# Kernel optimization log

Hardware: AMD Instinct MI355X
Metric: run time of the kernel (lower is better)

## Reference

```python
import jax, jax.numpy as jnp
import numpy as np

N_HEADS = 16
D_MODEL = 1024
D_HEAD = D_MODEL // N_HEADS


def setup_inputs() -> dict:
    key = jax.random.key(0)
    ks = jax.random.split(key, 5)
    scale = 0.02
    x = jax.random.normal(ks[0], (2, 2048, D_MODEL), dtype=jnp.float32)
    # torch.nn.Linear weights: (out_features, in_features)
    w_in = jax.random.normal(ks[1], (3 * D_MODEL, D_MODEL), dtype=jnp.float32) * scale
    b_in = jax.random.normal(ks[2], (3 * D_MODEL,), dtype=jnp.float32) * scale
    w_out = jax.random.normal(ks[3], (D_MODEL, D_MODEL), dtype=jnp.float32) * scale
    b_out = jax.random.normal(ks[4], (D_MODEL,), dtype=jnp.float32) * scale
    return {"x": x, "w_in": w_in, "b_in": b_in, "w_out": w_out, "b_out": b_out}


def reference(x, w_in, b_in, w_out, b_out):
    B, S, D = x.shape
    H, Dh = N_HEADS, D_HEAD
    qkv = x @ w_in.T + b_in                      # [B,S,3D]
    q, k, v = jnp.split(qkv, 3, axis=-1)
    q = q.reshape(B, S, H, Dh).transpose(0, 2, 1, 3)  # [B,H,S,Dh]
    k = k.reshape(B, S, H, Dh).transpose(0, 2, 1, 3)
    v = v.reshape(B, S, H, Dh).transpose(0, 2, 1, 3)
    scores = jnp.einsum('bhqd,bhkd->bhqk', q, k) / jnp.sqrt(jnp.float32(Dh))
    weights = jax.nn.softmax(scores, axis=-1)
    out = jnp.einsum('bhqk,bhkd->bhqd', weights, v)   # [B,H,S,Dh]
    # Faithful to original: reshape WITHOUT transposing heads back
    out = out.reshape(B, S, D)
    return out @ w_out.T + b_out
```

## Files before the change

kernel.cpp:

```cpp
#include <hip/hip_runtime.h>
#include <math.h>

constexpr int D_MODEL = 1024;
constexpr int N_HEADS = 16;
constexpr int D_HEAD  = 64;
constexpr int SEQ     = 2048;
constexpr int BATCH   = 2;
constexpr int M_ROWS  = BATCH * SEQ;
constexpr int QKV_N   = 3 * D_MODEL;
constexpr int KDIM    = 1024;
constexpr int NROWS   = BATCH * N_HEADS * SEQ;

typedef __bf16 bf16x8 __attribute__((ext_vector_type(8)));
typedef float  f32x4  __attribute__((ext_vector_type(4)));
typedef float  f32x16 __attribute__((ext_vector_type(16)));
typedef unsigned uint2v __attribute__((ext_vector_type(2)));

union U4 { uint4 u; bf16x8 b; ushort s[8]; };
union U2 { uint2 u; ushort s[4]; };

__device__ __forceinline__ unsigned pk2bf(float lo, float hi) {
    union { unsigned u; __bf16 b[2]; } cv;
    cv.b[0] = (__bf16)lo; cv.b[1] = (__bf16)hi;
    return cv.u;
}
__device__ __forceinline__ ushort f2bf(float f) {
    union { ushort s[2]; __bf16 b[2]; } cv;
    cv.b[0] = (__bf16)f;
    return cv.s[0];
}

__device__ __forceinline__ int swz(int row, int bytecol) {
    return row * 128 + (bytecol ^ ((row & 7) << 4));
}

__device__ __forceinline__ void gload16(const void* g, void* l) {
    __builtin_amdgcn_global_load_lds(
        (const __attribute__((address_space(1))) unsigned int*)g,
        (__attribute__((address_space(3))) unsigned int*)l, 16, 0, 0);
}

#define QSCALE 0.18033688011112042f

__global__ __launch_bounds__(256)
void convert3_kernel(const float* __restrict__ x,  ushort* __restrict__ xo,
                     const float* __restrict__ wi, ushort* __restrict__ wio,
                     const float* __restrict__ wo, ushort* __restrict__ woo) {
    const int na = M_ROWS * D_MODEL;
    const int nb = QKV_N * D_MODEL;
    const int nc = D_MODEL * D_MODEL;
    const int total = (na + nb + nc) / 8;
    for (int g = blockIdx.x * blockDim.x + threadIdx.x; g < total;
         g += gridDim.x * blockDim.x) {
        const int i = g * 8;
        const float* src; ushort* dst; int off;
        if (i < na)           { src = x;  dst = xo;  off = i; }
        else if (i < na + nb) { src = wi; dst = wio; off = i - na; }
        else                  { src = wo; dst = woo; off = i - na - nb; }
        const float4 a = *reinterpret_cast<const float4*>(src + off);
        const float4 b = *reinterpret_cast<const float4*>(src + off + 4);
        uint4 o;
        o.x = pk2bf(a.x, a.y); o.y = pk2bf(a.z, a.w);
        o.z = pk2bf(b.x, b.y); o.w = pk2bf(b.z, b.w);
        *reinterpret_cast<uint4*>(dst + off) = o;
    }
}

__device__ __forceinline__ void mfma_gemm_bt_128(
    const ushort* __restrict__ Ag, const ushort* __restrict__ Bg,
    int m0, int n0, ushort* As, ushort* Bs, f32x4 (&acc)[4][4])
{
    const int tid = threadIdx.x;
    const int l   = tid & 63;
    const int rl  = l & 15, hh = l >> 4;
    const int w   = tid >> 6;
    const int wm  = (w >> 1) * 64, wn = (w & 1) * 64;

    const int r0 = tid >> 2;
    const int ce = (tid & 3) * 8;
    const ushort* gA0 = Ag + (size_t)(m0 + r0) * KDIM + ce;
    const ushort* gA1 = gA0 + (size_t)64 * KDIM;
    const ushort* gB0 = Bg + (size_t)(n0 + r0) * KDIM + ce;
    const ushort* gB1 = gB0 + (size_t)64 * KDIM;
    char* lA = (char*)As + tid * 16;
    char* lB = (char*)Bs + tid * 16;

    for (int k0 = 0; k0 < KDIM; k0 += 32) {
        __syncthreads();
        gload16(gA0 + k0, lA);
        gload16(gA1 + k0, lA + 4096);
        gload16(gB0 + k0, lB);
        gload16(gB1 + k0, lB + 4096);
        __syncthreads();

        bf16x8 af[4], bf_[4];
        #pragma unroll
        for (int f = 0; f < 4; ++f)
            af[f]  = *(const bf16x8*)((const char*)As + (wm + f * 16 + rl) * 64 + hh * 16);
        #pragma unroll
        for (int f = 0; f < 4; ++f)
            bf_[f] = *(const bf16x8*)((const char*)Bs + (wn + f * 16 + rl) * 64 + hh * 16);
        #pragma unroll
        for (int i = 0; i < 4; ++i)
            #pragma unroll
            for (int j = 0; j < 4; ++j)
                acc[i][j] = __builtin_amdgcn_mfma_f32_16x16x32_bf16(af[i], bf_[j], acc[i][j], 0, 0, 0);
    }
}

__global__ __launch_bounds__(256)
void qkv_mfma_kernel(const ushort* __restrict__ xb, const ushort* __restrict__ wb,
                     const float* __restrict__ b_in,
                     ushort* __restrict__ Q, ushort* __restrict__ K, ushort* __restrict__ V) {
    __shared__ __align__(16) ushort As[128 * 32];
    __shared__ __align__(16) ushort Bs[128 * 32];

    f32x4 acc[4][4];
    #pragma unroll
    for (int i = 0; i < 4; ++i)
        #pragma unroll
        for (int j = 0; j < 4; ++j) acc[i][j] = (f32x4){0.f, 0.f, 0.f, 0.f};

    const int m0 = blockIdx.y * 128, n0 = blockIdx.x * 128;
    mfma_gemm_bt_128(xb, wb, m0, n0, As, Bs, acc);

    const int l  = threadIdx.x & 63, w = threadIdx.x >> 6;
    const int rl = l & 15, hh = l >> 4;
    const int mb = m0 + (w >> 1) * 64, nb = n0 + (w & 1) * 64;

    #pragma unroll
    for (int j = 0; j < 4; ++j) {
        const int n  = nb + j * 16 + rl;
        const float bias = b_in[n];
        const int t  = n >> 10;
        const int jj = n & 1023;
        const int h  = jj >> 6;
        const int d  = jj & 63;
        ushort* dst = (t == 0) ? Q : (t == 1) ? K : V;
        const float sc = (t == 0) ? QSCALE : 1.0f;
        #pragma unroll
        for (int i = 0; i < 4; ++i)
            #pragma unroll
            for (int r = 0; r < 4; ++r) {
                const int m = mb + i * 16 + hh * 4 + r;
                const int b = m >> 11;
                const int s = m & (SEQ - 1);
                dst[((size_t)(b * N_HEADS + h) * SEQ + s) * D_HEAD + d] =
                    f2bf((acc[i][j][r] + bias) * sc);
            }
    }
}

__global__ __launch_bounds__(512)
void attn_mfma_split_kernel(const ushort* __restrict__ Q, const ushort* __restrict__ K,
                            const ushort* __restrict__ V, ushort* __restrict__ Op,
                            float* __restrict__ lbuf) {
    __shared__ __align__(16) char Ks[2][64 * 128];
    __shared__ __align__(16) char Vs[2][64 * 128];

    const int tid = threadIdx.x;
    const int w   = tid >> 6;
    const int l   = tid & 63;
    const int l31 = l & 31;
    const int lh  = l >> 5;

    const int bid  = blockIdx.x;
    const int nid  = (bid & 7) * 64 + (bid >> 3);
    const int bh   = nid >> 4;
    const int rem  = nid & 15;
    const int half = rem >> 3;
    const int qt   = rem & 7;

    const size_t base  = (size_t)bh * SEQ * D_HEAD;
    const size_t kbase = base + (size_t)half * 1024 * D_HEAD;
    const int qbase = qt * 256 + w * 32;

    bf16x8 qf[4];
    {
        const ushort* qp = Q + base + (size_t)(qbase + l31) * D_HEAD + lh * 8;
        #pragma unroll
        for (int c = 0; c < 4; ++c) {
            U4 t; t.u = *(const uint4*)(qp + c * 16);
            qf[c] = t.b;
        }
    }

    f32x16 ot0, ot1;
    #pragma unroll
    for (int r = 0; r < 16; ++r) { ot0[r] = 0.f; ot1[r] = 0.f; }
    float l_run = 0.0f;

    const int sr  = tid >> 3, seg = tid & 7;
    const int kp  = (tid & 31) * 2, dc = (tid >> 5) * 4;
    const ushort* gK  = K + kbase + (size_t)sr * D_HEAD + seg * 8;
    const ushort* gV0 = V + kbase + (size_t)kp * D_HEAD + dc;
    const ushort* gV1 = gV0 + D_HEAD;

    uint4 ka; U2 va, vb;
    ka   = *(const uint4*)(gK);
    va.u = *(const uint2*)(gV0);
    vb.u = *(const uint2*)(gV1);
    {
        char* kd = Ks[0]; char* vd = Vs[0];
        *(uint4*)(kd + swz(sr, seg * 16)) = ka;
        #pragma unroll
        for (int i = 0; i < 4; ++i) {
            const int d = dc + i;
            *(unsigned*)(vd + d * 128 + ((kp * 2) ^ ((d & 7) << 4))) =
                (unsigned)va.s[i] | ((unsigned)vb.s[i] << 16);
        }
    }

    constexpr int NT = 1024 / 64;
    for (int t = 0; t < NT; ++t) {
        const int cur = t & 1;
        __syncthreads();

        if (t + 1 < NT) {
            const size_t off = (size_t)(t + 1) * 64 * D_HEAD;
            ka   = *(const uint4*)(gK + off);
            va.u = *(const uint2*)(gV0 + off);
            vb.u = *(const uint2*)(gV1 + off);
        }
        const char* kbuf = Ks[cur];
        const char* vbuf = Vs[cur];

        f32x16 st0, st1;
        #pragma unroll
        for (int r = 0; r < 16; ++r) { st0[r] = 0.f; st1[r] = 0.f; }
        #pragma unroll
        for (int c = 0; c < 4; ++c) {
            const bf16x8 kf0 = *(const bf16x8*)(kbuf + swz(l31,      c * 32 + lh * 16));
            st0 = __builtin_amdgcn_mfma_f32_32x32x16_bf16(kf0, qf[c], st0, 0, 0, 0);
            const bf16x8 kf1 = *(const bf16x8*)(kbuf + swz(32 + l31, c * 32 + lh * 16));
            st1 = __builtin_amdgcn_mfma_f32_32x32x16_bf16(kf1, qf[c], st1, 0, 0, 0);
        }

        float ps = 0.f;
        #pragma unroll
        for (int r = 0; r < 16; ++r) {
            st0[r] = __builtin_amdgcn_exp2f(st0[r]); ps += st0[r];
            st1[r] = __builtin_amdgcn_exp2f(st1[r]); ps += st1[r];
        }
        l_run += ps;

        bf16x8 paf[4];
        #pragma unroll
        for (int t32 = 0; t32 < 2; ++t32) {
            const f32x16& s = t32 ? st1 : st0;
            const unsigned q0 = pk2bf(s[0],  s[1]);
            const unsigned q1 = pk2bf(s[2],  s[3]);
            const unsigned q2 = pk2bf(s[4],  s[5]);
            const unsigned q3 = pk2bf(s[6],  s[7]);
            const unsigned q4 = pk2bf(s[8],  s[9]);
            const unsigned q5 = pk2bf(s[10], s[11]);
            const unsigned q6 = pk2bf(s[12], s[13]);
            const unsigned q7 = pk2bf(s[14], s[15]);
            const uint2v x = __builtin_amdgcn_permlane32_swap(q0, q2, false, false);
            const uint2v y = __builtin_amdgcn_permlane32_swap(q1, q3, false, false);
            const uint2v z = __builtin_amdgcn_permlane32_swap(q4, q6, false, false);
            const uint2v u = __builtin_amdgcn_permlane32_swap(q5, q7, false, false);
            U4 f0; f0.u.x = x[0]; f0.u.y = y[0]; f0.u.z = x[1]; f0.u.w = y[1];
            U4 f1; f1.u.x = z[0]; f1.u.y = u[0]; f1.u.z = z[1]; f1.u.w = u[1];
            paf[t32 * 2]     = f0.b;
            paf[t32 * 2 + 1] = f1.b;
        }

        #pragma unroll
        for (int kc = 0; kc < 4; ++kc) {
            const bf16x8 vf0 = *(const bf16x8*)(vbuf + swz(l31,      kc * 32 + lh * 16));
            ot0 = __builtin_amdgcn_mfma_f32_32x32x16_bf16(vf0, paf[kc], ot0, 0, 0, 0);
            const bf16x8 vf1 = *(const bf16x8*)(vbuf + swz(32 + l31, kc * 32 + lh * 16));
            ot1 = __builtin_amdgcn_mfma_f32_32x32x16_bf16(vf1, paf[kc], ot1, 0, 0, 0);
        }

        if (t + 1 < NT) {
            char* kd = Ks[cur ^ 1]; char* vd = Vs[cur ^ 1];
            *(uint4*)(kd + swz(sr, seg * 16)) = ka;
            #pragma unroll
            for (int i = 0; i < 4; ++i) {
                const int d = dc + i;
                *(unsigned*)(vd + d * 128 + ((kp * 2) ^ ((d & 7) << 4))) =
                    (unsigned)va.s[i] | ((unsigned)vb.s[i] << 16);
            }
        }
    }

    l_run += __shfl_xor(l_run, 32, 64);
    const size_t grow = (size_t)bh * SEQ + qbase + l31;
    ushort* op = Op + ((size_t)half * NROWS + grow) * D_HEAD;
    #pragma unroll
    for (int dt = 0; dt < 2; ++dt) {
        const f32x16& o = dt ? ot1 : ot0;
        #pragma unroll
        for (int g = 0; g < 4; ++g) {
            const int d0 = dt * 32 + g * 8 + lh * 4;
            uint2 s2;
            s2.x = pk2bf(o[g * 4 + 0], o[g * 4 + 1]);
            s2.y = pk2bf(o[g * 4 + 2], o[g * 4 + 3]);
            *(uint2*)(op + d0) = s2;
        }
    }
    if (lh == 0) lbuf[(size_t)half * NROWS + grow] = l_run;
}

__global__ __launch_bounds__(256)
void combine_kernel(const ushort* __restrict__ Op, const float* __restrict__ lbuf,
                    ushort* __restrict__ A) {
    const int idx = blockIdx.x * 256 + threadIdx.x;
    const int row = idx >> 3;
    const int dc  = (idx & 7) * 8;
    const float inv = 1.0f / (lbuf[row] + lbuf[NROWS + row]);
    U4 o1, o2;
    o1.u = *(const uint4*)(Op + (size_t)row * D_HEAD + dc);
    o2.u = *(const uint4*)(Op + ((size_t)NROWS + row) * D_HEAD + dc);
    uint4 r;
    float v[8];
    #pragma unroll
    for (int i = 0; i < 8; ++i)
        v[i] = ((float)o1.b[i] + (float)o2.b[i]) * inv;
    r.x = pk2bf(v[0], v[1]); r.y = pk2bf(v[2], v[3]);
    r.z = pk2bf(v[4], v[5]); r.w = pk2bf(v[6], v[7]);
    *(uint4*)(A + (size_t)row * D_HEAD + dc) = r;
}

__global__ __launch_bounds__(256)
void out_mfma_kernel(const ushort* __restrict__ Ab, const ushort* __restrict__ wb,
                     const float* __restrict__ b_out, float* __restrict__ out) {
    __shared__ __align__(16) ushort As[128 * 32];
    __shared__ __align__(16) ushort Bs[128 * 32];

    f32x4 acc[4][4];
    #pragma unroll
    for (int i = 0; i < 4; ++i)
        #pragma unroll
        for (int j = 0; j < 4; ++j) acc[i][j] = (f32x4){0.f, 0.f, 0.f, 0.f};

    const int m0 = blockIdx.y * 128, n0 = blockIdx.x * 128;
    mfma_gemm_bt_128(Ab, wb, m0, n0, As, Bs, acc);

    const int l  = threadIdx.x & 63, w = threadIdx.x >> 6;
    const int rl = l & 15, hh = l >> 4;
    const int mb = m0 + (w >> 1) * 64, nb = n0 + (w & 1) * 64;

    #pragma unroll
    for (int j = 0; j < 4; ++j) {
        const int n = nb + j * 16 + rl;
        const float bias = b_out[n];
        #pragma unroll
        for (int i = 0; i < 4; ++i)
            #pragma unroll
            for (int r = 0; r < 4; ++r) {
                const int m = mb + i * 16 + hh * 4 + r;
                out[(size_t)m * D_MODEL + n] = acc[i][j][r] + bias;
            }
    }
}

extern "C" void kernel_launch(void* const* d_in, const int* in_sizes, int n_in,
                              void* d_out, int out_size, void* d_ws, size_t ws_size,
                              hipStream_t stream) {
    const float* x     = (const float*)d_in[0];
    const float* w_in  = (const float*)d_in[1];
    const float* b_in  = (const float*)d_in[2];
    const float* w_out = (const float*)d_in[3];
    const float* b_out = (const float*)d_in[4];
    float* out = (float*)d_out;

    const size_t T = (size_t)BATCH * N_HEADS * SEQ * D_HEAD;
    ushort* Qw  = (ushort*)d_ws;
    ushort* Kw  = Qw + T;
    ushort* Vw  = Kw + T;
    ushort* Opw = Vw + T;
    ushort* xb  = Opw + T;
    ushort* wib = xb + T;
    ushort* wob = wib + (size_t)QKV_N * D_MODEL;
    float*  lw  = (float*)(wob + (size_t)D_MODEL * D_MODEL);
    ushort* Aw  = Qw;

    convert3_kernel<<<2048, 256, 0, stream>>>(x, xb, w_in, wib, w_out, wob);

    qkv_mfma_kernel<<<dim3(QKV_N / 128, M_ROWS / 128), 256, 0, stream>>>(
        xb, wib, b_in, Qw, Kw, Vw);
    attn_mfma_split_kernel<<<512, 512, 0, stream>>>(Qw, Kw, Vw, Opw, lw);
    combine_kernel<<<NROWS * 8 / 256, 256, 0, stream>>>(Opw, lw, Aw);
    out_mfma_kernel<<<dim3(D_MODEL / 128, M_ROWS / 128), 256, 0, stream>>>(
        Aw, wob, b_out, out);
}
```

Before: 125.3 us.

## Fuse split-attention combine into output GEMM and interleave softmax with PV MFMAs

Removes the separate combine kernel. The output projection GEMM now loads both partial attention outputs, normalizes them by the summed row denominators, and writes the result straight into its shared-memory A tile, with the next tile prefetched into registers. This drops one launch and one round trip of the attention output through global memory, but each GEMM block repeats the combine work for its tile and issues extra loads. Inside the attention loop, the exp and PV MFMAs for the two 32-key halves are interleaved with s_setprio hints so that VALU work on one half can overlap the matrix ops on the other.

```diff
diff --git a/kernel.cpp b/kernel.cpp
--- a/kernel.cpp
+++ b/kernel.cpp
@@ -228,51 +228,103 @@
         f32x16 st0, st1;
         #pragma unroll
         for (int r = 0; r < 16; ++r) { st0[r] = 0.f; st1[r] = 0.f; }
+        __builtin_amdgcn_s_setprio(1);
         #pragma unroll
         for (int c = 0; c < 4; ++c) {
-            const bf16x8 kf0 = *(const bf16x8*)(kbuf + swz(l31,      c * 32 + lh * 16));
+            const bf16x8 kf0 = *(const bf16x8*)(kbuf + swz(l31, c * 32 + lh * 16));
             st0 = __builtin_amdgcn_mfma_f32_32x32x16_bf16(kf0, qf[c], st0, 0, 0, 0);
+        }
+        #pragma unroll
+        for (int c = 0; c < 4; ++c) {
             const bf16x8 kf1 = *(const bf16x8*)(kbuf + swz(32 + l31, c * 32 + lh * 16));
             st1 = __builtin_amdgcn_mfma_f32_32x32x16_bf16(kf1, qf[c], st1, 0, 0, 0);
         }
-
-        float ps = 0.f;
-        #pragma unroll
-        for (int r = 0; r < 16; ++r) {
-            st0[r] = __builtin_amdgcn_exp2f(st0[r]); ps += st0[r];
-            st1[r] = __builtin_amdgcn_exp2f(st1[r]); ps += st1[r];
-        }
-        l_run += ps;
-
-        bf16x8 paf[4];
-        #pragma unroll
-        for (int t32 = 0; t32 < 2; ++t32) {
-            const f32x16& s = t32 ? st1 : st0;
-            const unsigned q0 = pk2bf(s[0],  s[1]);
-            const unsigned q1 = pk2bf(s[2],  s[3]);
-            const unsigned q2 = pk2bf(s[4],  s[5]);
-            const unsigned q3 = pk2bf(s[6],  s[7]);
-            const unsigned q4 = pk2bf(s[8],  s[9]);
-            const unsigned q5 = pk2bf(s[10], s[11]);
-            const unsigned q6 = pk2bf(s[12], s[13]);
-            const unsigned q7 = pk2bf(s[14], s[15]);
+        __builtin_amdgcn_s_setprio(0);
+
+        float p0a = 0.f, p0b = 0.f, p0c = 0.f, p0d = 0.f;
+        #pragma unroll
+        for (int r = 0; r < 4; ++r) {
+            st0[r]      = __builtin_amdgcn_exp2f(st0[r]);      p0a += st0[r];
+            st0[4 + r]  = __builtin_amdgcn_exp2f(st0[4 + r]);  p0b += st0[4 + r];
+            st0[8 + r]  = __builtin_amdgcn_exp2f(st0[8 + r]);  p0c += st0[8 + r];
+            st0[12 + r] = __builtin_amdgcn_exp2f(st0[12 + r]); p0d += st0[12 + r];
+        }
+        const float ps0 = (p0a + p0b) + (p0c + p0d);
+
+        bf16x8 paf0, paf1;
+        {
+            const unsigned q0 = pk2bf(st0[0],  st0[1]);
+            const unsigned q1 = pk2bf(st0[2],  st0[3]);
+            const unsigned q2 = pk2bf(st0[4],  st0[5]);
+            const unsigned q3 = pk2bf(st0[6],  st0[7]);
+            const unsigned q4 = pk2bf(st0[8],  st0[9]);
+            const unsigned q5 = pk2bf(st0[10], st0[11]);
+            const unsigned q6 = pk2bf(st0[12], st0[13]);
+            const unsigned q7 = pk2bf(st0[14], st0[15]);
             const uint2v x = __builtin_amdgcn_permlane32_swap(q0, q2, false, false);
             const uint2v y = __builtin_amdgcn_permlane32_swap(q1, q3, false, false);
             const uint2v z = __builtin_amdgcn_permlane32_swap(q4, q6, false, false);
             const uint2v u = __builtin_amdgcn_permlane32_swap(q5, q7, false, false);
             U4 f0; f0.u.x = x[0]; f0.u.y = y[0]; f0.u.z = x[1]; f0.u.w = y[1];
             U4 f1; f1.u.x = z[0]; f1.u.y = u[0]; f1.u.z = z[1]; f1.u.w = u[1];
-            paf[t32 * 2]     = f0.b;
-            paf[t32 * 2 + 1] = f1.b;
-        }
-
-        #pragma unroll
-        for (int kc = 0; kc < 4; ++kc) {
-            const bf16x8 vf0 = *(const bf16x8*)(vbuf + swz(l31,      kc * 32 + lh * 16));
-            ot0 = __builtin_amdgcn_mfma_f32_32x32x16_bf16(vf0, paf[kc], ot0, 0, 0, 0);
-            const bf16x8 vf1 = *(const bf16x8*)(vbuf + swz(32 + l31, kc * 32 + lh * 16));
-            ot1 = __builtin_amdgcn_mfma_f32_32x32x16_bf16(vf1, paf[kc], ot1, 0, 0, 0);
-        }
+            paf0 = f0.b; paf1 = f1.b;
+        }
+
+        __builtin_amdgcn_s_setprio(1);
+        {
+            const bf16x8 vf0 = *(const bf16x8*)(vbuf + swz(l31,      0 * 32 + lh * 16));
+            ot0 = __builtin_amdgcn_mfma_f32_32x32x16_bf16(vf0, paf0, ot0, 0, 0, 0);
+            const bf16x8 vf1 = *(const bf16x8*)(vbuf + swz(32 + l31, 0 * 32 + lh * 16));
+            ot1 = __builtin_amdgcn_mfma_f32_32x32x16_bf16(vf1, paf0, ot1, 0, 0, 0);
+            const bf16x8 vf2 = *(const bf16x8*)(vbuf + swz(l31,      1 * 32 + lh * 16));
+            ot0 = __builtin_amdgcn_mfma_f32_32x32x16_bf16(vf2, paf1, ot0, 0, 0, 0);
+            const bf16x8 vf3 = *(const bf16x8*)(vbuf + swz(32 + l31, 1 * 32 + lh * 16));
+            ot1 = __builtin_amdgcn_mfma_f32_32x32x16_bf16(vf3, paf1, ot1, 0, 0, 0);
+        }
+        __builtin_amdgcn_s_setprio(0);
+
+        float p1a = 0.f, p1b = 0.f, p1c = 0.f, p1d = 0.f;
+        #pragma unroll
+        for (int r = 0; r < 4; ++r) {
+            st1[r]      = __builtin_amdgcn_exp2f(st1[r]);      p1a += st1[r];
+            st1[4 + r]  = __builtin_amdgcn_exp2f(st1[4 + r]);  p1b += st1[4 + r];
+            st1[8 + r]  = __builtin_amdgcn_exp2f(st1[8 + r]);  p1c += st1[8 + r];
+            st1[12 + r] = __builtin_amdgcn_exp2f(st1[12 + r]); p1d += st1[12 + r];
+        }
+        const float ps1 = (p1a + p1b) + (p1c + p1d);
+        l_run += ps0 + ps1;
+
+        bf16x8 paf2, paf3;
+        {
+            const unsigned q0 = pk2bf(st1[0],  st1[1]);
+            const unsigned q1 = pk2bf(st1[2],  st1[3]);
+            const unsigned q2 = pk2bf(st1[4],  st1[5]);
+            const unsigned q3 = pk2bf(st1[6],  st1[7]);
+            const unsigned q4 = pk2bf(st1[8],  st1[9]);
+            const unsigned q5 = pk2bf(st1[10], st1[11]);
+            const unsigned q6 = pk2bf(st1[12], st1[13]);
+            const unsigned q7 = pk2bf(st1[14], st1[15]);
+            const uint2v x = __builtin_amdgcn_permlane32_swap(q0, q2, false, false);
+            const uint2v y = __builtin_amdgcn_permlane32_swap(q1, q3, false, false);
+            const uint2v z = __builtin_amdgcn_permlane32_swap(q4, q6, false, false);
+            const uint2v u = __builtin_amdgcn_permlane32_swap(q5, q7, false, false);
+            U4 f0; f0.u.x = x[0]; f0.u.y = y[0]; f0.u.z = x[1]; f0.u.w = y[1];
+            U4 f1; f1.u.x = z[0]; f1.u.y = u[0]; f1.u.z = z[1]; f1.u.w = u[1];
+            paf2 = f0.b; paf3 = f1.b;
+        }
+
+        __builtin_amdgcn_s_setprio(1);
+        {
+            const bf16x8 vf0 = *(const bf16x8*)(vbuf + swz(l31,      2 * 32 + lh * 16));
+            ot0 = __builtin_amdgcn_mfma_f32_32x32x16_bf16(vf0, paf2, ot0, 0, 0, 0);
+            const bf16x8 vf1 = *(const bf16x8*)(vbuf + swz(32 + l31, 2 * 32 + lh * 16));
+            ot1 = __builtin_amdgcn_mfma_f32_32x32x16_bf16(vf1, paf2, ot1, 0, 0, 0);
+            const bf16x8 vf2 = *(const bf16x8*)(vbuf + swz(l31,      3 * 32 + lh * 16));
+            ot0 = __builtin_amdgcn_mfma_f32_32x32x16_bf16(vf2, paf3, ot0, 0, 0, 0);
+            const bf16x8 vf3 = *(const bf16x8*)(vbuf + swz(32 + l31, 3 * 32 + lh * 16));
+            ot1 = __builtin_amdgcn_mfma_f32_32x32x16_bf16(vf3, paf3, ot1, 0, 0, 0);
+        }
+        __builtin_amdgcn_s_setprio(0);
 
         if (t + 1 < NT) {
             char* kd = Ks[cur ^ 1]; char* vd = Vs[cur ^ 1];
@@ -304,45 +356,101 @@
     if (lh == 0) lbuf[(size_t)half * NROWS + grow] = l_run;
 }
 
-__global__ __launch_bounds__(256)
-void combine_kernel(const ushort* __restrict__ Op, const float* __restrict__ lbuf,
-                    ushort* __restrict__ A) {
-    const int idx = blockIdx.x * 256 + threadIdx.x;
-    const int row = idx >> 3;
-    const int dc  = (idx & 7) * 8;
-    const float inv = 1.0f / (lbuf[row] + lbuf[NROWS + row]);
-    U4 o1, o2;
-    o1.u = *(const uint4*)(Op + (size_t)row * D_HEAD + dc);
-    o2.u = *(const uint4*)(Op + ((size_t)NROWS + row) * D_HEAD + dc);
+__device__ __forceinline__ uint4 comb8(U4 a, U4 b, float inv) {
+    float v[8];
+    #pragma unroll
+    for (int i = 0; i < 8; ++i)
+        v[i] = ((float)a.b[i] + (float)b.b[i]) * inv;
     uint4 r;
-    float v[8];
-    #pragma unroll
-    for (int i = 0; i < 8; ++i)
-        v[i] = ((float)o1.b[i] + (float)o2.b[i]) * inv;
     r.x = pk2bf(v[0], v[1]); r.y = pk2bf(v[2], v[3]);
     r.z = pk2bf(v[4], v[5]); r.w = pk2bf(v[6], v[7]);
-    *(uint4*)(A + (size_t)row * D_HEAD + dc) = r;
+    return r;
 }
 
 __global__ __launch_bounds__(256)
-void out_mfma_kernel(const ushort* __restrict__ Ab, const ushort* __restrict__ wb,
-                     const float* __restrict__ b_out, float* __restrict__ out) {
+void out_mfma_kernel(const ushort* __restrict__ Op, const float* __restrict__ lbuf,
+                     const ushort* __restrict__ wb, const float* __restrict__ b_out,
+                     float* __restrict__ out) {
     __shared__ __align__(16) ushort As[128 * 32];
     __shared__ __align__(16) ushort Bs[128 * 32];
 
+    const int tid = threadIdx.x;
+    const int l   = tid & 63;
+    const int rl  = l & 15, hh = l >> 4;
+    const int w   = tid >> 6;
+    const int wm  = (w >> 1) * 64, wn = (w & 1) * 64;
+    const int m0  = blockIdx.y * 128, n0 = blockIdx.x * 128;
+
+    const int r0 = tid >> 2;
+    const int ce = (tid & 3) * 8;
+    const ushort* gB0 = wb + (size_t)(n0 + r0) * KDIM + ce;
+    const ushort* gB1 = gB0 + (size_t)64 * KDIM;
+    char* lA = (char*)As + tid * 16;
+    char* lB = (char*)Bs + tid * 16;
+
+    const ushort* OpB  = Op + (size_t)NROWS * D_HEAD;
+    const size_t row0  = (size_t)(m0 + r0) * KDIM;
+    const size_t row1  = row0 + (size_t)64 * KDIM;
+    const int g0base = (m0 + r0) * 16;
+    const int g1base = g0base + 64 * 16;
+
     f32x4 acc[4][4];
     #pragma unroll
     for (int i = 0; i < 4; ++i)
         #pragma unroll
         for (int j = 0; j < 4; ++j) acc[i][j] = (f32x4){0.f, 0.f, 0.f, 0.f};
 
-    const int m0 = blockIdx.y * 128, n0 = blockIdx.x * 128;
-    mfma_gemm_bt_128(Ab, wb, m0, n0, As, Bs, acc);
-
-    const int l  = threadIdx.x & 63, w = threadIdx.x >> 6;
-    const int rl = l & 15, hh = l >> 4;
+    uint4 w0v, w1v;
+    {
+        const int k  = ce;
+        const int gb = k >> 6;
+        const float inv0 = 1.0f / (lbuf[g0base + gb] + lbuf[NROWS + g0base + gb]);
+        const float inv1 = 1.0f / (lbuf[g1base + gb] + lbuf[NROWS + g1base + gb]);
+        U4 a, b, c, d;
+        a.u = *(const uint4*)(Op  + row0 + k);
+        b.u = *(const uint4*)(OpB + row0 + k);
+        c.u = *(const uint4*)(Op  + row1 + k);
+        d.u = *(const uint4*)(OpB + row1 + k);
+        w0v = comb8(a, b, inv0);
+        w1v = comb8(c, d, inv1);
+    }
+
+    for (int k0 = 0; k0 < KDIM; k0 += 32) {
+        __syncthreads();
+        gload16(gB0 + k0, lB);
+        gload16(gB1 + k0, lB + 4096);
+        *(uint4*)lA          = w0v;
+        *(uint4*)(lA + 4096) = w1v;
+        if (k0 + 32 < KDIM) {
+            const int k  = k0 + 32 + ce;
+            const int gb = k >> 6;
+            const float inv0 = 1.0f / (lbuf[g0base + gb] + lbuf[NROWS + g0base + gb]);
+            const float inv1 = 1.0f / (lbuf[g1base + gb] + lbuf[NROWS + g1base + gb]);
+            U4 a, b, c, d;
+            a.u = *(const uint4*)(Op  + row0 + k);
+            b.u = *(const uint4*)(OpB + row0 + k);
+            c.u = *(const uint4*)(Op  + row1 + k);
+            d.u = *(const uint4*)(OpB + row1 + k);
+            w0v = comb8(a, b, inv0);
+            w1v = comb8(c, d, inv1);
+        }
+        __syncthreads();
+
+        bf16x8 af[4], bf_[4];
+        #pragma unroll
+        for (int f = 0; f < 4; ++f)
+            af[f]  = *(const bf16x8*)((const char*)As + (wm + f * 16 + rl) * 64 + hh * 16);
+        #pragma unroll
+        for (int f = 0; f < 4; ++f)
+            bf_[f] = *(const bf16x8*)((const char*)Bs + (wn + f * 16 + rl) * 64 + hh * 16);
+        #pragma unroll
+        for (int i = 0; i < 4; ++i)
+            #pragma unroll
+            for (int j = 0; j < 4; ++j)
+                acc[i][j] = __builtin_amdgcn_mfma_f32_16x16x32_bf16(af[i], bf_[j], acc[i][j], 0, 0, 0);
+    }
+
     const int mb = m0 + (w >> 1) * 64, nb = n0 + (w & 1) * 64;
-
     #pragma unroll
     for (int j = 0; j < 4; ++j) {
         const int n = nb + j * 16 + rl;
@@ -376,14 +484,12 @@
     ushort* wib = xb + T;
     ushort* wob = wib + (size_t)QKV_N * D_MODEL;
     float*  lw  = (float*)(wob + (size_t)D_MODEL * D_MODEL);
-    ushort* Aw  = Qw;
 
     convert3_kernel<<<2048, 256, 0, stream>>>(x, xb, w_in, wib, w_out, wob);
 
     qkv_mfma_kernel<<<dim3(QKV_N / 128, M_ROWS / 128), 256, 0, stream>>>(
         xb, wib, b_in, Qw, Kw, Vw);
     attn_mfma_split_kernel<<<512, 512, 0, stream>>>(Qw, Kw, Vw, Opw, lw);
-    combine_kernel<<<NROWS * 8 / 256, 256, 0, stream>>>(Opw, lw, Aw);
     out_mfma_kernel<<<dim3(D_MODEL / 128, M_ROWS / 128), 256, 0, stream>>>(
-        Aw, wob, b_out, out);
-}
+        Opw, lw, wob, b_out, out);
+}
```

New measurement: 154.3 us. 1.23x slower.

## Process two 32-row query tiles per wave in split attention kernel

Applied to the files above, without the earlier changes.

Each wave now handles 64 query rows, as two 32-row tiles, instead of 32. The block shrinks from 512 to 256 threads while keeping 256 query rows per block. Each K/V fragment read from LDS now feeds twice as many MFMAs, which halves LDS read traffic per unit of compute and lets each thread issue wider global loads. The cost is roughly double the accumulator and score registers per wave, which may lower occupancy or cause spills, and fewer waves are available to hide latency.

```diff
diff --git a/kernel.cpp b/kernel.cpp
--- a/kernel.cpp
+++ b/kernel.cpp
@@ -17,7 +17,6 @@
 typedef unsigned uint2v __attribute__((ext_vector_type(2)));
 
 union U4 { uint4 u; bf16x8 b; ushort s[8]; };
-union U2 { uint2 u; ushort s[4]; };
 
 __device__ __forceinline__ unsigned pk2bf(float lo, float hi) {
     union { unsigned u; __bf16 b[2]; } cv;
@@ -41,6 +40,24 @@
 }
 
 #define QSCALE 0.18033688011112042f
+
+__device__ __forceinline__ void pack_paf(const f32x16& s, bf16x8& f0o, bf16x8& f1o) {
+    const unsigned q0 = pk2bf(s[0],  s[1]);
+    const unsigned q1 = pk2bf(s[2],  s[3]);
+    const unsigned q2 = pk2bf(s[4],  s[5]);
+    const unsigned q3 = pk2bf(s[6],  s[7]);
+    const unsigned q4 = pk2bf(s[8],  s[9]);
+    const unsigned q5 = pk2bf(s[10], s[11]);
+    const unsigned q6 = pk2bf(s[12], s[13]);
+    const unsigned q7 = pk2bf(s[14], s[15]);
+    const uint2v x = __builtin_amdgcn_permlane32_swap(q0, q2, false, false);
+    const uint2v y = __builtin_amdgcn_permlane32_swap(q1, q3, false, false);
+    const uint2v z = __builtin_amdgcn_permlane32_swap(q4, q6, false, false);
+    const uint2v u = __builtin_amdgcn_permlane32_swap(q5, q7, false, false);
+    U4 f0; f0.u.x = x[0]; f0.u.y = y[0]; f0.u.z = x[1]; f0.u.w = y[1];
+    U4 f1; f1.u.x = z[0]; f1.u.y = u[0]; f1.u.z = z[1]; f1.u.w = u[1];
+    f0o = f0.b; f1o = f1.b;
+}
 
 __global__ __launch_bounds__(256)
 void convert3_kernel(const float* __restrict__ x,  ushort* __restrict__ xo,
@@ -151,7 +168,7 @@
     }
 }
 
-__global__ __launch_bounds__(512)
+__global__ __launch_bounds__(256)
 void attn_mfma_split_kernel(const ushort* __restrict__ Q, const ushort* __restrict__ K,
                             const ushort* __restrict__ V, ushort* __restrict__ Op,
                             float* __restrict__ lbuf) {
@@ -173,39 +190,42 @@
 
     const size_t base  = (size_t)bh * SEQ * D_HEAD;
     const size_t kbase = base + (size_t)half * 1024 * D_HEAD;
-    const int qbase = qt * 256 + w * 32;
-
-    bf16x8 qf[4];
+    const int qbase = qt * 256 + w * 64;
+
+    bf16x8 qfA[4], qfB[4];
     {
-        const ushort* qp = Q + base + (size_t)(qbase + l31) * D_HEAD + lh * 8;
+        const ushort* qpA = Q + base + (size_t)(qbase + l31) * D_HEAD + lh * 8;
+        const ushort* qpB = qpA + (size_t)32 * D_HEAD;
         #pragma unroll
         for (int c = 0; c < 4; ++c) {
-            U4 t; t.u = *(const uint4*)(qp + c * 16);
-            qf[c] = t.b;
-        }
-    }
-
-    f32x16 ot0, ot1;
-    #pragma unroll
-    for (int r = 0; r < 16; ++r) { ot0[r] = 0.f; ot1[r] = 0.f; }
-    float l_run = 0.0f;
-
-    const int sr  = tid >> 3, seg = tid & 7;
-    const int kp  = (tid & 31) * 2, dc = (tid >> 5) * 4;
+            U4 ta; ta.u = *(const uint4*)(qpA + c * 16); qfA[c] = ta.b;
+            U4 tb; tb.u = *(const uint4*)(qpB + c * 16); qfB[c] = tb.b;
+        }
+    }
+
+    f32x16 otA0, otA1, otB0, otB1;
+    #pragma unroll
+    for (int r = 0; r < 16; ++r) { otA0[r] = 0.f; otA1[r] = 0.f; otB0[r] = 0.f; otB1[r] = 0.f; }
+    float lA = 0.0f, lB = 0.0f;
+
+    const int sr  = tid >> 2, seg = tid & 3;
+    const int kp  = (tid & 31) * 2, db = tid >> 5;
     const ushort* gK  = K + kbase + (size_t)sr * D_HEAD + seg * 8;
-    const ushort* gV0 = V + kbase + (size_t)kp * D_HEAD + dc;
+    const ushort* gV0 = V + kbase + (size_t)kp * D_HEAD + db * 8;
     const ushort* gV1 = gV0 + D_HEAD;
 
-    uint4 ka; U2 va, vb;
+    uint4 ka, kb; U4 va, vb;
     ka   = *(const uint4*)(gK);
-    va.u = *(const uint2*)(gV0);
-    vb.u = *(const uint2*)(gV1);
+    kb   = *(const uint4*)(gK + 32);
+    va.u = *(const uint4*)(gV0);
+    vb.u = *(const uint4*)(gV1);
     {
         char* kd = Ks[0]; char* vd = Vs[0];
-        *(uint4*)(kd + swz(sr, seg * 16)) = ka;
-        #pragma unroll
-        for (int i = 0; i < 4; ++i) {
-            const int d = dc + i;
+        *(uint4*)(kd + swz(sr, seg * 16))      = ka;
+        *(uint4*)(kd + swz(sr, seg * 16 + 64)) = kb;
+        #pragma unroll
+        for (int i = 0; i < 8; ++i) {
+            const int d = db * 8 + i;
             *(unsigned*)(vd + d * 128 + ((kp * 2) ^ ((d & 7) << 4))) =
                 (unsigned)va.s[i] | ((unsigned)vb.s[i] << 16);
         }
@@ -219,89 +239,92 @@
         if (t + 1 < NT) {
             const size_t off = (size_t)(t + 1) * 64 * D_HEAD;
             ka   = *(const uint4*)(gK + off);
-            va.u = *(const uint2*)(gV0 + off);
-            vb.u = *(const uint2*)(gV1 + off);
+            kb   = *(const uint4*)(gK + off + 32);
+            va.u = *(const uint4*)(gV0 + off);
+            vb.u = *(const uint4*)(gV1 + off);
         }
         const char* kbuf = Ks[cur];
         const char* vbuf = Vs[cur];
 
-        f32x16 st0, st1;
-        #pragma unroll
-        for (int r = 0; r < 16; ++r) { st0[r] = 0.f; st1[r] = 0.f; }
+        f32x16 sA0, sA1, sB0, sB1;
+        #pragma unroll
+        for (int r = 0; r < 16; ++r) { sA0[r] = 0.f; sA1[r] = 0.f; sB0[r] = 0.f; sB1[r] = 0.f; }
         #pragma unroll
         for (int c = 0; c < 4; ++c) {
-            const bf16x8 kf0 = *(const bf16x8*)(kbuf + swz(l31,      c * 32 + lh * 16));
-            st0 = __builtin_amdgcn_mfma_f32_32x32x16_bf16(kf0, qf[c], st0, 0, 0, 0);
+            const bf16x8 kf0 = *(const bf16x8*)(kbuf + swz(l31, c * 32 + lh * 16));
+            sA0 = __builtin_amdgcn_mfma_f32_32x32x16_bf16(kf0, qfA[c], sA0, 0, 0, 0);
+            sB0 = __builtin_amdgcn_mfma_f32_32x32x16_bf16(kf0, qfB[c], sB0, 0, 0, 0);
             const bf16x8 kf1 = *(const bf16x8*)(kbuf + swz(32 + l31, c * 32 + lh * 16));
-            st1 = __builtin_amdgcn_mfma_f32_32x32x16_bf16(kf1, qf[c], st1, 0, 0, 0);
-        }
-
-        float ps = 0.f;
+            sA1 = __builtin_amdgcn_mfma_f32_32x32x16_bf16(kf1, qfA[c], sA1, 0, 0, 0);
+            sB1 = __builtin_amdgcn_mfma_f32_32x32x16_bf16(kf1, qfB[c], sB1, 0, 0, 0);
+        }
+
+        float psA = 0.f, psB = 0.f;
         #pragma unroll
         for (int r = 0; r < 16; ++r) {
-            st0[r] = __builtin_amdgcn_exp2f(st0[r]); ps += st0[r];
-            st1[r] = __builtin_amdgcn_exp2f(st1[r]); ps += st1[r];
-        }
-        l_run += ps;
-
-        bf16x8 paf[4];
-        #pragma unroll
-        for (int t32 = 0; t32 < 2; ++t32) {
-            const f32x16& s = t32 ? st1 : st0;
-            const unsigned q0 = pk2bf(s[0],  s[1]);
-            const unsigned q1 = pk2bf(s[2],  s[3]);
-            const unsigned q2 = pk2bf(s[4],  s[5]);
-            const unsigned q3 = pk2bf(s[6],  s[7]);
-            const unsigned q4 = pk2bf(s[8],  s[9]);
-            const unsigned q5 = pk2bf(s[10], s[11]);
-            const unsigned q6 = pk2bf(s[12], s[13]);
-            const unsigned q7 = pk2bf(s[14], s[15]);
-            const uint2v x = __builtin_amdgcn_permlane32_swap(q0, q2, false, false);
-            const uint2v y = __builtin_amdgcn_permlane32_swap(q1, q3, false, false);
-            const uint2v z = __builtin_amdgcn_permlane32_swap(q4, q6, false, false);
-            const uint2v u = __builtin_amdgcn_permlane32_swap(q5, q7, false, false);
-            U4 f0; f0.u.x = x[0]; f0.u.y = y[0]; f0.u.z = x[1]; f0.u.w = y[1];
-            U4 f1; f1.u.x = z[0]; f1.u.y = u[0]; f1.u.z = z[1]; f1.u.w = u[1];
-            paf[t32 * 2]     = f0.b;
-            paf[t32 * 2 + 1] = f1.b;
-        }
+            sA0[r] = __builtin_amdgcn_exp2f(sA0[r]); psA += sA0[r];
+            sA1[r] = __builtin_amdgcn_exp2f(sA1[r]); psA += sA1[r];
+            sB0[r] = __builtin_amdgcn_exp2f(sB0[r]); psB += sB0[r];
+            sB1[r] = __builtin_amdgcn_exp2f(sB1[r]); psB += sB1[r];
+        }
+        lA += psA; lB += psB;
+
+        bf16x8 pafA[4], pafB[4];
+        pack_paf(sA0, pafA[0], pafA[1]);
+        pack_paf(sA1, pafA[2], pafA[3]);
+        pack_paf(sB0, pafB[0], pafB[1]);
+        pack_paf(sB1, pafB[2], pafB[3]);
 
         #pragma unroll
         for (int kc = 0; kc < 4; ++kc) {
-            const bf16x8 vf0 = *(const bf16x8*)(vbuf + swz(l31,      kc * 32 + lh * 16));
-            ot0 = __builtin_amdgcn_mfma_f32_32x32x16_bf16(vf0, paf[kc], ot0, 0, 0, 0);
+            const bf16x8 vf0 = *(const bf16x8*)(vbuf + swz(l31, kc * 32 + lh * 16));
+            otA0 = __builtin_amdgcn_mfma_f32_32x32x16_bf16(vf0, pafA[kc], otA0, 0, 0, 0);
+            otB0 = __builtin_amdgcn_mfma_f32_32x32x16_bf16(vf0, pafB[kc], otB0, 0, 0, 0);
             const bf16x8 vf1 = *(const bf16x8*)(vbuf + swz(32 + l31, kc * 32 + lh * 16));
-            ot1 = __builtin_amdgcn_mfma_f32_32x32x16_bf16(vf1, paf[kc], ot1, 0, 0, 0);
+            otA1 = __builtin_amdgcn_mfma_f32_32x32x16_bf16(vf1, pafA[kc], otA1, 0, 0, 0);
+            otB1 = __builtin_amdgcn_mfma_f32_32x32x16_bf16(vf1, pafB[kc], otB1, 0, 0, 0);
         }
 
         if (t + 1 < NT) {
             char* kd = Ks[cur ^ 1]; char* vd = Vs[cur ^ 1];
-            *(uint4*)(kd + swz(sr, seg * 16)) = ka;
+            *(uint4*)(kd + swz(sr, seg * 16))      = ka;
+            *(uint4*)(kd + swz(sr, seg * 16 + 64)) = kb;
             #pragma unroll
-            for (int i = 0; i < 4; ++i) {
-                const int d = dc + i;
+            for (int i = 0; i < 8; ++i) {
+                const int d = db * 8 + i;
                 *(unsigned*)(vd + d * 128 + ((kp * 2) ^ ((d & 7) << 4))) =
                     (unsigned)va.s[i] | ((unsigned)vb.s[i] << 16);
             }
         }
     }
 
-    l_run += __shfl_xor(l_run, 32, 64);
-    const size_t grow = (size_t)bh * SEQ + qbase + l31;
-    ushort* op = Op + ((size_t)half * NROWS + grow) * D_HEAD;
+    lA += __shfl_xor(lA, 32, 64);
+    lB += __shfl_xor(lB, 32, 64);
+    const size_t growA = (size_t)bh * SEQ + qbase + l31;
+    const size_t growB = growA + 32;
+    ushort* opA = Op + ((size_t)half * NROWS + growA) * D_HEAD;
+    ushort* opB = Op + ((size_t)half * NROWS + growB) * D_HEAD;
     #pragma unroll
     for (int dt = 0; dt < 2; ++dt) {
-        const f32x16& o = dt ? ot1 : ot0;
+        const f32x16& oa = dt ? otA1 : otA0;
+        const f32x16& ob = dt ? otB1 : otB0;
         #pragma unroll
         for (int g = 0; g < 4; ++g) {
             const int d0 = dt * 32 + g * 8 + lh * 4;
             uint2 s2;
-            s2.x = pk2bf(o[g * 4 + 0], o[g * 4 + 1]);
-            s2.y = pk2bf(o[g * 4 + 2], o[g * 4 + 3]);
-            *(uint2*)(op + d0) = s2;
-        }
-    }
-    if (lh == 0) lbuf[(size_t)half * NROWS + grow] = l_run;
+            s2.x = pk2bf(oa[g * 4 + 0], oa[g * 4 + 1]);
+            s2.y = pk2bf(oa[g * 4 + 2], oa[g * 4 + 3]);
+            *(uint2*)(opA + d0) = s2;
+            uint2 s3;
+            s3.x = pk2bf(ob[g * 4 + 0], ob[g * 4 + 1]);
+            s3.y = pk2bf(ob[g * 4 + 2], ob[g * 4 + 3]);
+            *(uint2*)(opB + d0) = s3;
+        }
+    }
+    if (lh == 0) {
+        lbuf[(size_t)half * NROWS + growA] = lA;
+        lbuf[(size_t)half * NROWS + growB] = lB;
+    }
 }
 
 __global__ __launch_bounds__(256)
@@ -382,7 +405,7 @@
 
     qkv_mfma_kernel<<<dim3(QKV_N / 128, M_ROWS / 128), 256, 0, stream>>>(
         xb, wib, b_in, Qw, Kw, Vw);
-    attn_mfma_split_kernel<<<512, 512, 0, stream>>>(Qw, Kw, Vw, Opw, lw);
+    attn_mfma_split_kernel<<<512, 256, 0, stream>>>(Qw, Kw, Vw, Opw, lw);
     combine_kernel<<<NROWS * 8 / 256, 256, 0, stream>>>(Opw, lw, Aw);
     out_mfma_kernel<<<dim3(D_MODEL / 128, M_ROWS / 128), 256, 0, stream>>>(
         Aw, wob, b_out, out);
```

Result: slower. 136.6 us (+9.0%).

## Write V pre-transposed from QKV GEMM and stream K/V via direct global-to-LDS loads

Applied to the files above, without the earlier changes.

The QKV projection epilogue now stages V tiles in shared memory and writes V transposed ([b,h,d,s]) with coalesced 16-byte stores. The attention kernel can then fetch both K and V tiles with global_load_lds directly into swizzled LDS, with no register staging and no per-element transpose scatter into shared memory. This removes the register round-trip and the strided V loads from the attention inner loop, at the cost of extra LDS use (about 34 KB) and a barrier in the QKV kernel. It also relies on the async LDS loads being complete at the next __syncthreads.

```diff
diff --git a/kernel.cpp b/kernel.cpp
--- a/kernel.cpp
+++ b/kernel.cpp
@@ -17,7 +17,6 @@
 typedef unsigned uint2v __attribute__((ext_vector_type(2)));
 
 union U4 { uint4 u; bf16x8 b; ushort s[8]; };
-union U2 { uint2 u; ushort s[4]; };
 
 __device__ __forceinline__ unsigned pk2bf(float lo, float hi) {
     union { unsigned u; __bf16 b[2]; } cv;
@@ -41,6 +40,24 @@
 }
 
 #define QSCALE 0.18033688011112042f
+
+__device__ __forceinline__ void pack_paf(const f32x16& s, bf16x8& f0o, bf16x8& f1o) {
+    const unsigned q0 = pk2bf(s[0],  s[1]);
+    const unsigned q1 = pk2bf(s[2],  s[3]);
+    const unsigned q2 = pk2bf(s[4],  s[5]);
+    const unsigned q3 = pk2bf(s[6],  s[7]);
+    const unsigned q4 = pk2bf(s[8],  s[9]);
+    const unsigned q5 = pk2bf(s[10], s[11]);
+    const unsigned q6 = pk2bf(s[12], s[13]);
+    const unsigned q7 = pk2bf(s[14], s[15]);
+    const uint2v x = __builtin_amdgcn_permlane32_swap(q0, q2, false, false);
+    const uint2v y = __builtin_amdgcn_permlane32_swap(q1, q3, false, false);
+    const uint2v z = __builtin_amdgcn_permlane32_swap(q4, q6, false, false);
+    const uint2v u = __builtin_amdgcn_permlane32_swap(q5, q7, false, false);
+    U4 f0; f0.u.x = x[0]; f0.u.y = y[0]; f0.u.z = x[1]; f0.u.w = y[1];
+    U4 f1; f1.u.x = z[0]; f1.u.y = u[0]; f1.u.z = z[1]; f1.u.w = u[1];
+    f0o = f0.b; f1o = f1.b;
+}
 
 __global__ __launch_bounds__(256)
 void convert3_kernel(const float* __restrict__ x,  ushort* __restrict__ xo,
@@ -114,6 +131,7 @@
                      ushort* __restrict__ Q, ushort* __restrict__ K, ushort* __restrict__ V) {
     __shared__ __align__(16) ushort As[128 * 32];
     __shared__ __align__(16) ushort Bs[128 * 32];
+    __shared__ __align__(16) ushort VT[128 * 136];
 
     f32x4 acc[4][4];
     #pragma unroll
@@ -124,36 +142,65 @@
     const int m0 = blockIdx.y * 128, n0 = blockIdx.x * 128;
     mfma_gemm_bt_128(xb, wb, m0, n0, As, Bs, acc);
 
-    const int l  = threadIdx.x & 63, w = threadIdx.x >> 6;
+    const int tid = threadIdx.x;
+    const int l  = tid & 63, w = tid >> 6;
     const int rl = l & 15, hh = l >> 4;
     const int mb = m0 + (w >> 1) * 64, nb = n0 + (w & 1) * 64;
 
-    #pragma unroll
-    for (int j = 0; j < 4; ++j) {
-        const int n  = nb + j * 16 + rl;
-        const float bias = b_in[n];
-        const int t  = n >> 10;
-        const int jj = n & 1023;
-        const int h  = jj >> 6;
-        const int d  = jj & 63;
-        ushort* dst = (t == 0) ? Q : (t == 1) ? K : V;
-        const float sc = (t == 0) ? QSCALE : 1.0f;
-        #pragma unroll
-        for (int i = 0; i < 4; ++i)
+    if (n0 < 2048) {
+        ushort* dst = (n0 < 1024) ? Q : K;
+        const float sc = (n0 < 1024) ? QSCALE : 1.0f;
+        #pragma unroll
+        for (int j = 0; j < 4; ++j) {
+            const int n  = nb + j * 16 + rl;
+            const float bias = b_in[n];
+            const int jj = n & 1023;
+            const int h  = jj >> 6;
+            const int d  = jj & 63;
             #pragma unroll
-            for (int r = 0; r < 4; ++r) {
-                const int m = mb + i * 16 + hh * 4 + r;
-                const int b = m >> 11;
-                const int s = m & (SEQ - 1);
-                dst[((size_t)(b * N_HEADS + h) * SEQ + s) * D_HEAD + d] =
-                    f2bf((acc[i][j][r] + bias) * sc);
+            for (int i = 0; i < 4; ++i)
+                #pragma unroll
+                for (int r = 0; r < 4; ++r) {
+                    const int m = mb + i * 16 + hh * 4 + r;
+                    const int b = m >> 11;
+                    const int s = m & (SEQ - 1);
+                    dst[((size_t)(b * N_HEADS + h) * SEQ + s) * D_HEAD + d] =
+                        f2bf((acc[i][j][r] + bias) * sc);
+                }
+        }
+    } else {
+        #pragma unroll
+        for (int j = 0; j < 4; ++j) {
+            const int nl = (w & 1) * 64 + j * 16 + rl;
+            const float bias = b_in[n0 + nl];
+            #pragma unroll
+            for (int i = 0; i < 4; ++i) {
+                const int mc = (w >> 1) * 64 + i * 16 + hh * 4;
+                uint2 p;
+                p.x = pk2bf(acc[i][j][0] + bias, acc[i][j][1] + bias);
+                p.y = pk2bf(acc[i][j][2] + bias, acc[i][j][3] + bias);
+                *(uint2*)&VT[nl * 136 + mc] = p;
             }
+        }
+        __syncthreads();
+        const int b   = m0 >> 11;
+        const int s0  = m0 & (SEQ - 1);
+        const int jj0 = n0 - 2048;
+        const int chunk = tid & 15, r0 = tid >> 4;
+        #pragma unroll
+        for (int rr = 0; rr < 8; ++rr) {
+            const int nl = r0 + rr * 16;
+            const int h  = (jj0 + nl) >> 6;
+            const int d  = (jj0 + nl) & 63;
+            const uint4 v = *(const uint4*)&VT[nl * 136 + chunk * 8];
+            *(uint4*)(V + ((size_t)(b * N_HEADS + h) * D_HEAD + d) * SEQ + s0 + chunk * 8) = v;
+        }
     }
 }
 
 __global__ __launch_bounds__(512)
 void attn_mfma_split_kernel(const ushort* __restrict__ Q, const ushort* __restrict__ K,
-                            const ushort* __restrict__ V, ushort* __restrict__ Op,
+                            const ushort* __restrict__ Vt_g, ushort* __restrict__ Op,
                             float* __restrict__ lbuf) {
     __shared__ __align__(16) char Ks[2][64 * 128];
     __shared__ __align__(16) char Vs[2][64 * 128];
@@ -171,8 +218,7 @@
     const int half = rem >> 3;
     const int qt   = rem & 7;
 
-    const size_t base  = (size_t)bh * SEQ * D_HEAD;
-    const size_t kbase = base + (size_t)half * 1024 * D_HEAD;
+    const size_t base = (size_t)bh * SEQ * D_HEAD;
     const int qbase = qt * 256 + w * 32;
 
     bf16x8 qf[4];
@@ -190,26 +236,13 @@
     for (int r = 0; r < 16; ++r) { ot0[r] = 0.f; ot1[r] = 0.f; }
     float l_run = 0.0f;
 
-    const int sr  = tid >> 3, seg = tid & 7;
-    const int kp  = (tid & 31) * 2, dc = (tid >> 5) * 4;
-    const ushort* gK  = K + kbase + (size_t)sr * D_HEAD + seg * 8;
-    const ushort* gV0 = V + kbase + (size_t)kp * D_HEAD + dc;
-    const ushort* gV1 = gV0 + D_HEAD;
-
-    uint4 ka; U2 va, vb;
-    ka   = *(const uint4*)(gK);
-    va.u = *(const uint2*)(gV0);
-    vb.u = *(const uint2*)(gV1);
-    {
-        char* kd = Ks[0]; char* vd = Vs[0];
-        *(uint4*)(kd + swz(sr, seg * 16)) = ka;
-        #pragma unroll
-        for (int i = 0; i < 4; ++i) {
-            const int d = dc + i;
-            *(unsigned*)(vd + d * 128 + ((kp * 2) ^ ((d & 7) << 4))) =
-                (unsigned)va.s[i] | ((unsigned)vb.s[i] << 16);
-        }
-    }
+    const int srow = tid >> 3, schunk = tid & 7;
+    const int cg = schunk ^ (srow & 7);
+    const ushort* gK = K    + base + (size_t)(half * 1024 + srow) * D_HEAD + cg * 8;
+    const ushort* gV = Vt_g + base + (size_t)srow * SEQ + half * 1024 + cg * 8;
+
+    gload16(gK, Ks[0] + tid * 16);
+    gload16(gV, Vs[0] + tid * 16);
 
     constexpr int NT = 1024 / 64;
     for (int t = 0; t < NT; ++t) {
@@ -217,10 +250,8 @@
         __syncthreads();
 
         if (t + 1 < NT) {
-            const size_t off = (size_t)(t + 1) * 64 * D_HEAD;
-            ka   = *(const uint4*)(gK + off);
-            va.u = *(const uint2*)(gV0 + off);
-            vb.u = *(const uint2*)(gV1 + off);
+            gload16(gK + (size_t)(t + 1) * 64 * D_HEAD, Ks[cur ^ 1] + tid * 16);
+            gload16(gV + (t + 1) * 64,                  Vs[cur ^ 1] + tid * 16);
         }
         const char* kbuf = Ks[cur];
         const char* vbuf = Vs[cur];
@@ -245,26 +276,8 @@
         l_run += ps;
 
         bf16x8 paf[4];
-        #pragma unroll
-        for (int t32 = 0; t32 < 2; ++t32) {
-            const f32x16& s = t32 ? st1 : st0;
-            const unsigned q0 = pk2bf(s[0],  s[1]);
-            const unsigned q1 = pk2bf(s[2],  s[3]);
-            const unsigned q2 = pk2bf(s[4],  s[5]);
-            const unsigned q3 = pk2bf(s[6],  s[7]);
-            const unsigned q4 = pk2bf(s[8],  s[9]);
-            const unsigned q5 = pk2bf(s[10], s[11]);
-            const unsigned q6 = pk2bf(s[12], s[13]);
-            const unsigned q7 = pk2bf(s[14], s[15]);
-            const uint2v x = __builtin_amdgcn_permlane32_swap(q0, q2, false, false);
-            const uint2v y = __builtin_amdgcn_permlane32_swap(q1, q3, false, false);
-            const uint2v z = __builtin_amdgcn_permlane32_swap(q4, q6, false, false);
-            const uint2v u = __builtin_amdgcn_permlane32_swap(q5, q7, false, false);
-            U4 f0; f0.u.x = x[0]; f0.u.y = y[0]; f0.u.z = x[1]; f0.u.w = y[1];
-            U4 f1; f1.u.x = z[0]; f1.u.y = u[0]; f1.u.z = z[1]; f1.u.w = u[1];
-            paf[t32 * 2]     = f0.b;
-            paf[t32 * 2 + 1] = f1.b;
-        }
+        pack_paf(st0, paf[0], paf[1]);
+        pack_paf(st1, paf[2], paf[3]);
 
         #pragma unroll
         for (int kc = 0; kc < 4; ++kc) {
@@ -272,17 +285,6 @@
             ot0 = __builtin_amdgcn_mfma_f32_32x32x16_bf16(vf0, paf[kc], ot0, 0, 0, 0);
             const bf16x8 vf1 = *(const bf16x8*)(vbuf + swz(32 + l31, kc * 32 + lh * 16));
             ot1 = __builtin_amdgcn_mfma_f32_32x32x16_bf16(vf1, paf[kc], ot1, 0, 0, 0);
-        }
-
-        if (t + 1 < NT) {
-            char* kd = Ks[cur ^ 1]; char* vd = Vs[cur ^ 1];
-            *(uint4*)(kd + swz(sr, seg * 16)) = ka;
-            #pragma unroll
-            for (int i = 0; i < 4; ++i) {
-                const int d = dc + i;
-                *(unsigned*)(vd + d * 128 + ((kp * 2) ^ ((d & 7) << 4))) =
-                    (unsigned)va.s[i] | ((unsigned)vb.s[i] << 16);
-            }
         }
     }
 
```

Result: slower. 146.4 us (+16.8%).
